# Kernel tuning notes

Hardware: AMD Instinct MI355X
Metric: run time of the kernel (lower is better)

The kernel has to match this reference:

```python
import jax, jax.numpy as jnp
import numpy as np

C = 128      # in channels
CO = 64      # out channels
G = 32       # group-norm groups
RES_IN = 32  # input resolution
RES_OUT = 64 # subdivided resolution
N = 20000    # active input voxels
EPS = 1e-5


def setup_inputs() -> dict:
    key = jax.random.key(0)
    ks = jax.random.split(key, 12)
    # unique active voxel coords at RES_IN (batch index 0, single instance)
    rng = np.random.default_rng(0)
    flat = rng.choice(RES_IN ** 3, size=N, replace=False)
    xyz = np.stack([flat // (RES_IN * RES_IN), (flat // RES_IN) % RES_IN, flat % RES_IN], axis=1)
    x_coords = jnp.asarray(np.concatenate([np.zeros((N, 1), np.int32), xyz.astype(np.int32)], axis=1))
    x_feats = jax.random.normal(ks[0], (N, C), dtype=jnp.float32)
    gn1_g = 1.0 + 0.1 * jax.random.normal(ks[1], (C,), dtype=jnp.float32)
    gn1_b = 0.1 * jax.random.normal(ks[2], (C,), dtype=jnp.float32)
    W1 = 0.05 * jax.random.normal(ks[3], (3, 3, 3, C, CO), dtype=jnp.float32)
    b1 = 0.01 * jax.random.normal(ks[4], (CO,), dtype=jnp.float32)
    gn2_g = 1.0 + 0.1 * jax.random.normal(ks[5], (CO,), dtype=jnp.float32)
    gn2_b = 0.1 * jax.random.normal(ks[6], (CO,), dtype=jnp.float32)
    W2 = 0.05 * jax.random.normal(ks[7], (3, 3, 3, CO, CO), dtype=jnp.float32)  # zero_module in source; random here to exercise math
    b2 = 0.01 * jax.random.normal(ks[8], (CO,), dtype=jnp.float32)
    Ws = 0.05 * jax.random.normal(ks[9], (C, CO), dtype=jnp.float32)   # 1x1 skip conv
    bs = 0.01 * jax.random.normal(ks[10], (CO,), dtype=jnp.float32)
    return dict(x_feats=x_feats, x_coords=x_coords, gn1_g=gn1_g, gn1_b=gn1_b,
                W1=W1, b1=b1, gn2_g=gn2_g, gn2_b=gn2_b, W2=W2, b2=b2, Ws=Ws, bs=bs)


def group_norm(f, g, b):
    # single-instance sparse group norm: stats per group over all points
    n, c = f.shape
    x = f.reshape(n, G, c // G)
    mu = jnp.mean(x, axis=(0, 2), keepdims=True)
    var = jnp.mean((x - mu) ** 2, axis=(0, 2), keepdims=True)
    return ((x - mu) * jax.lax.rsqrt(var + EPS)).reshape(n, c) * g + b


def subdivide(coords, feats):
    n = coords.shape[0]
    offs = jnp.stack(jnp.meshgrid(jnp.arange(2), jnp.arange(2), jnp.arange(2), indexing='ij'), -1).reshape(8, 3)
    xyz = coords[:, None, 1:] * 2 + offs[None].astype(coords.dtype)          # [n,8,3]
    bidx = jnp.broadcast_to(coords[:, None, :1], (n, 8, 1))
    new_coords = jnp.concatenate([bidx, xyz], axis=-1).reshape(n * 8, 4)
    return new_coords, jnp.repeat(feats, 8, axis=0)


def subm_conv3(coords, feats, W, b):
    # submanifold 3x3x3 sparse conv: scatter to padded dense grid, gather 27 neighbors per active site
    cin = feats.shape[1]
    grid = jnp.zeros((RES_OUT + 2, RES_OUT + 2, RES_OUT + 2, cin), feats.dtype)
    grid = grid.at[coords[:, 1] + 1, coords[:, 2] + 1, coords[:, 3] + 1].set(feats)
    acc = jnp.zeros((feats.shape[0], W.shape[-1]), feats.dtype)
    for i in range(3):
        for j in range(3):
            for k in range(3):
                nb = grid[coords[:, 1] + i, coords[:, 2] + j, coords[:, 3] + k]  # [n, cin]
                acc = acc + nb @ W[i, j, k]
    return acc + b


def reference(x_feats, x_coords, gn1_g, gn1_b, W1, b1, gn2_g, gn2_b, W2, b2, Ws, bs):
    h = jax.nn.silu(group_norm(x_feats, gn1_g, gn1_b))
    hc, hf = subdivide(x_coords, h)
    _, xf = subdivide(x_coords, x_feats)
    hf = subm_conv3(hc, hf, W1, b1)
    hf = jax.nn.silu(group_norm(hf, gn2_g, gn2_b))
    hf = subm_conv3(hc, hf, W2, b2)
    out = hf + (xf @ Ws + bs)  # residual + 1x1 skip conv (out_channels != channels)
    return out
```

## Files before the change

### kernel.cpp

```cpp
#include <hip/hip_runtime.h>
#include <hip/hip_bf16.h>
#include <math.h>

#define N_PTS 20000
#define C_IN 128
#define C_OUT 64
#define M_PTS (N_PTS*8)
#define EPS 1e-5f

typedef __attribute__((ext_vector_type(8))) short short8;
typedef __attribute__((ext_vector_type(4))) float float4v;

__device__ __forceinline__ ushort f2bf(float f){
    unsigned int i = __float_as_uint(f);
    unsigned int r = i + 0x7fffu + ((i >> 16) & 1u);
    return (ushort)(r >> 16);
}
__device__ __forceinline__ float bf2f(ushort u){ return __uint_as_float(((unsigned int)u) << 16); }
__device__ __forceinline__ float silu(float z){ return z / (1.f + expf(-z)); }


__global__ void __launch_bounds__(256) prep_kernel(
    const float* __restrict__ W1, const float* __restrict__ W2,
    ushort* __restrict__ Wt1, ushort* __restrict__ Wt2,
    int* __restrict__ pg, ushort* __restrict__ h, ushort* __restrict__ h2,
    const float* __restrict__ x, float* __restrict__ stats)
{
    const int b = blockIdx.x, tid = threadIdx.x;
    if (b < 864){
        int idx = b * 256 + tid;
        int j = idx & 7, l = (idx >> 3) & 63, nb = (idx >> 9) & 3, kb = (idx >> 11) & 3, t = idx >> 13;
        int ci = kb * 32 + (l >> 4) * 8 + j, co = nb * 16 + (l & 15);
        Wt1[idx] = f2bf(W1[(t * C_IN + ci) * 64 + co]);
    } else if (b < 1296){
        int idx = (b - 864) * 256 + tid;
        int j = idx & 7, l = (idx >> 3) & 63, nb = (idx >> 9) & 3, kb = (idx >> 11) & 1, t = idx >> 12;
        int ci = kb * 32 + (l >> 4) * 8 + j, co = nb * 16 + (l & 15);
        Wt2[idx] = f2bf(W2[(t * C_OUT + ci) * 64 + co]);
    } else if (b < 1424){
        int i = (b - 1296) * 256 + tid;
        pg[i] = -1;
        if (b == 1296){
            if (tid < C_IN) h[(size_t)N_PTS * C_IN + tid] = 0;
            if (tid < C_OUT) h2[(size_t)M_PTS * C_OUT + tid] = 0;
        }
    } else {
        __shared__ float ls[64];
        if (tid < 64) ls[tid] = 0.f;
        __syncthreads();
        const int g = tid & 31;
        const int r0 = (b - 1424) * 8 + (tid >> 5);
        float sum = 0.f, sq = 0.f;
        for (int r = r0; r < N_PTS; r += 4096){
            float4 v = *(const float4*)(x + (size_t)r * C_IN + g * 4);
            sum += v.x + v.y + v.z + v.w;
            sq  += v.x*v.x + v.y*v.y + v.z*v.z + v.w*v.w;
        }
        atomicAdd(&ls[g], sum);
        atomicAdd(&ls[32 + g], sq);
        __syncthreads();
        if (tid < 64) atomicAdd(&stats[tid], ls[tid]);
    }
}

__global__ void __launch_bounds__(256) mid_kernel(
    const int* __restrict__ cds, int* __restrict__ pg,
    const float* __restrict__ x, const float* __restrict__ stats,
    const float* __restrict__ g1, const float* __restrict__ b1, ushort* __restrict__ h,
    const float* __restrict__ Wsk, const float* __restrict__ bsk, float* __restrict__ s)
{
    __shared__ float w[C_IN * C_OUT];
    const int b = blockIdx.x, tid = threadIdx.x;
    if (b < 79){
        int i = b * 256 + tid;
        if (i < N_PTS){
            const int* cd = cds + i * 4;
            pg[(cd[1] * 32 + cd[2]) * 32 + cd[3]] = i;
        }
    } else if (b < 2579){
        int i = ((b - 79) * 256 + tid) * 4;
        int c0 = i & (C_IN - 1);
        int g = c0 >> 2;
        float mu = stats[g] * (1.0f / (N_PTS * 4.0f));
        float var = stats[32 + g] * (1.0f / (N_PTS * 4.0f)) - mu * mu;
        float rs = rsqrtf(var + EPS);
        float4 v = *(const float4*)(x + i);
        ushort4 o;
        o.x = f2bf(silu((v.x - mu) * rs * g1[c0+0] + b1[c0+0]));
        o.y = f2bf(silu((v.y - mu) * rs * g1[c0+1] + b1[c0+1]));
        o.z = f2bf(silu((v.z - mu) * rs * g1[c0+2] + b1[c0+2]));
        o.w = f2bf(silu((v.w - mu) * rs * g1[c0+3] + b1[c0+3]));
        *(ushort4*)(h + i) = o;
    } else {
        for (int j = tid; j < C_IN * C_OUT; j += 256) w[j] = Wsk[j];
        __syncthreads();
        int co = tid & 63, pr = tid >> 6;
        int p = (b - 2579) * 4 + pr;
        const float* xr = x + (size_t)p * C_IN;
        float a = bsk[co];
        for (int cb = 0; cb < C_IN; cb += 4){
            float4 v = *(const float4*)(xr + cb);
            a += v.x * w[(cb+0)*64+co] + v.y * w[(cb+1)*64+co]
               + v.z * w[(cb+2)*64+co] + v.w * w[(cb+3)*64+co];
        }
        s[(size_t)p * C_OUT + co] = a;
    }
}

template<int CIN, int CHILD>
__global__ void __launch_bounds__(64, 3) conv_direct(
    const ushort* __restrict__ feat, const int* __restrict__ pg,
    const int* __restrict__ coords, const ushort* __restrict__ Wt,
    const float* __restrict__ bias, const float* __restrict__ skip,
    ushort* __restrict__ hf1_bf, float* __restrict__ out, float* __restrict__ statsAcc)
{
    constexpr int KB = CIN / 32;
    __shared__ int rws[64];
    const int l = threadIdx.x;
    const int r16 = l & 15, qd = l >> 4;
    const int mb = blockIdx.x * 64;

    int cx0, cy0, cz0;
    {
        int m = mb + l, p = m >> 3, o = m & 7;
        cx0 = 2 * coords[p*4+1] + ((o >> 2) & 1);
        cy0 = 2 * coords[p*4+2] + ((o >> 1) & 1);
        cz0 = 2 * coords[p*4+3] + (o & 1);
    }

    float4v acc[4][4];
#pragma unroll
    for (int rb = 0; rb < 4; rb++)
#pragma unroll
        for (int nb = 0; nb < 4; nb++)
#pragma unroll
            for (int rg = 0; rg < 4; rg++) acc[rb][nb][rg] = 0.f;

    for (int t = 0; t < 27; t++){
        const int dx = t / 9 - 1, dy = (t / 3) % 3 - 1, dz = t % 3 - 1;
        const int cx = cx0 + dx, cy = cy0 + dy, cz = cz0 + dz;
        int row = 8 * N_PTS;
        if ((unsigned)cx < 64u && (unsigned)cy < 64u && (unsigned)cz < 64u){
            int pidx = pg[((cx >> 1) * 32 + (cy >> 1)) * 32 + (cz >> 1)];
            if (pidx >= 0) row = pidx * 8 + (((cx & 1) << 2) | ((cy & 1) << 1) | (cz & 1));
        }
        rws[l] = row;
        __syncthreads();
        int fr0 = rws[r16], fr1 = rws[16 + r16], fr2 = rws[32 + r16], fr3 = rws[48 + r16];
        if (!CHILD){ fr0 >>= 3; fr1 >>= 3; fr2 >>= 3; fr3 >>= 3; }
        const ushort* a0 = feat + (size_t)fr0 * CIN + qd * 8;
        const ushort* a1 = feat + (size_t)fr1 * CIN + qd * 8;
        const ushort* a2 = feat + (size_t)fr2 * CIN + qd * 8;
        const ushort* a3 = feat + (size_t)fr3 * CIN + qd * 8;
        const ushort* wt = Wt + (size_t)t * (KB * 2048) + l * 8;
#pragma unroll
        for (int kb = 0; kb < KB; kb++){
            short8 b0 = *(const short8*)(wt + (kb*4+0)*512);
            short8 b1 = *(const short8*)(wt + (kb*4+1)*512);
            short8 b2 = *(const short8*)(wt + (kb*4+2)*512);
            short8 b3 = *(const short8*)(wt + (kb*4+3)*512);
            short8 av0 = *(const short8*)(a0 + kb*32);
            short8 av1 = *(const short8*)(a1 + kb*32);
            short8 av2 = *(const short8*)(a2 + kb*32);
            short8 av3 = *(const short8*)(a3 + kb*32);
            acc[0][0] = __builtin_amdgcn_mfma_f32_16x16x32_bf16(av0, b0, acc[0][0], 0, 0, 0);
            acc[0][1] = __builtin_amdgcn_mfma_f32_16x16x32_bf16(av0, b1, acc[0][1], 0, 0, 0);
            acc[0][2] = __builtin_amdgcn_mfma_f32_16x16x32_bf16(av0, b2, acc[0][2], 0, 0, 0);
            acc[0][3] = __builtin_amdgcn_mfma_f32_16x16x32_bf16(av0, b3, acc[0][3], 0, 0, 0);
            acc[1][0] = __builtin_amdgcn_mfma_f32_16x16x32_bf16(av1, b0, acc[1][0], 0, 0, 0);
            acc[1][1] = __builtin_amdgcn_mfma_f32_16x16x32_bf16(av1, b1, acc[1][1], 0, 0, 0);
            acc[1][2] = __builtin_amdgcn_mfma_f32_16x16x32_bf16(av1, b2, acc[1][2], 0, 0, 0);
            acc[1][3] = __builtin_amdgcn_mfma_f32_16x16x32_bf16(av1, b3, acc[1][3], 0, 0, 0);
            acc[2][0] = __builtin_amdgcn_mfma_f32_16x16x32_bf16(av2, b0, acc[2][0], 0, 0, 0);
            acc[2][1] = __builtin_amdgcn_mfma_f32_16x16x32_bf16(av2, b1, acc[2][1], 0, 0, 0);
            acc[2][2] = __builtin_amdgcn_mfma_f32_16x16x32_bf16(av2, b2, acc[2][2], 0, 0, 0);
            acc[2][3] = __builtin_amdgcn_mfma_f32_16x16x32_bf16(av2, b3, acc[2][3], 0, 0, 0);
            acc[3][0] = __builtin_amdgcn_mfma_f32_16x16x32_bf16(av3, b0, acc[3][0], 0, 0, 0);
            acc[3][1] = __builtin_amdgcn_mfma_f32_16x16x32_bf16(av3, b1, acc[3][1], 0, 0, 0);
            acc[3][2] = __builtin_amdgcn_mfma_f32_16x16x32_bf16(av3, b2, acc[3][2], 0, 0, 0);
            acc[3][3] = __builtin_amdgcn_mfma_f32_16x16x32_bf16(av3, b3, acc[3][3], 0, 0, 0);
        }
    }

    float bsv[4] = { bias[r16], bias[16 + r16], bias[32 + r16], bias[48 + r16] };
    if (!CHILD){
        float ps[4] = {0,0,0,0}, pq[4] = {0,0,0,0};
#pragma unroll
        for (int rb = 0; rb < 4; rb++)
#pragma unroll
            for (int nb = 0; nb < 4; nb++)
#pragma unroll
                for (int rg = 0; rg < 4; rg++){
                    int mm = mb + rb * 16 + qd * 4 + rg;
                    float v = acc[rb][nb][rg] + bsv[nb];
                    hf1_bf[(size_t)mm * 64 + nb * 16 + r16] = f2bf(v);
                    ps[nb] += v; pq[nb] += v * v;
                }
#pragma unroll
        for (int nb = 0; nb < 4; nb++){
            float s1 = ps[nb], s2 = pq[nb];
            s1 += __shfl_xor(s1, 16, 64); s2 += __shfl_xor(s2, 16, 64);
            s1 += __shfl_xor(s1, 32, 64); s2 += __shfl_xor(s2, 32, 64);
            if (qd == 0){
                atomicAdd(&statsAcc[64 + nb * 16 + r16], s1);
                atomicAdd(&statsAcc[128 + nb * 16 + r16], s2);
            }
        }
    } else {
#pragma unroll
        for (int rb = 0; rb < 4; rb++)
#pragma unroll
            for (int rg = 0; rg < 4; rg++){
                int mm = mb + rb * 16 + qd * 4 + rg;
                const float* sk = skip + (size_t)(mm >> 3) * 64;
#pragma unroll
                for (int nb = 0; nb < 4; nb++){
                    int co = nb * 16 + r16;
                    out[(size_t)mm * 64 + co] = acc[rb][nb][rg] + bsv[nb] + sk[co];
                }
            }
    }
}

__global__ void __launch_bounds__(256) h2_kernel(
    const ushort* __restrict__ hf1, const float* __restrict__ stats,
    const float* __restrict__ gg, const float* __restrict__ gb, ushort* __restrict__ h2)
{
    int i = (blockIdx.x * 256 + threadIdx.x) * 4;
    if (i >= M_PTS * C_OUT) return;
    int c0 = i & (C_OUT - 1);
    const float inv = 1.0f / (M_PTS * 2.0f);
    float muA = (stats[64 + c0] + stats[64 + c0 + 1]) * inv;
    float vA  = (stats[128 + c0] + stats[128 + c0 + 1]) * inv - muA * muA;
    float rsA = rsqrtf(vA + EPS);
    float muB = (stats[64 + c0 + 2] + stats[64 + c0 + 3]) * inv;
    float vB  = (stats[128 + c0 + 2] + stats[128 + c0 + 3]) * inv - muB * muB;
    float rsB = rsqrtf(vB + EPS);
    ushort4 u = *(const ushort4*)(hf1 + i);
    ushort4 o;
    o.x = f2bf(silu((bf2f(u.x) - muA) * rsA * gg[c0+0] + gb[c0+0]));
    o.y = f2bf(silu((bf2f(u.y) - muA) * rsA * gg[c0+1] + gb[c0+1]));
    o.z = f2bf(silu((bf2f(u.z) - muB) * rsB * gg[c0+2] + gb[c0+2]));
    o.w = f2bf(silu((bf2f(u.w) - muB) * rsB * gg[c0+3] + gb[c0+3]));
    *(ushort4*)(h2 + i) = o;
}

extern "C" void kernel_launch(void* const* d_in, const int* in_sizes, int n_in,
                              void* d_out, int out_size, void* d_ws, size_t ws_size,
                              hipStream_t stream){
    const float* x   = (const float*)d_in[0];
    const int*   cds = (const int*)  d_in[1];
    const float* g1  = (const float*)d_in[2];
    const float* b1  = (const float*)d_in[3];
    const float* W1  = (const float*)d_in[4];
    const float* bb1 = (const float*)d_in[5];
    const float* g2  = (const float*)d_in[6];
    const float* b2  = (const float*)d_in[7];
    const float* W2  = (const float*)d_in[8];
    const float* bb2 = (const float*)d_in[9];
    const float* Wsk = (const float*)d_in[10];
    const float* bsk = (const float*)d_in[11];
    float* out = (float*)d_out;
    char* ws = (char*)d_ws;

    float*  stats = (float*) (ws);
    int*    pg    = (int*)   (ws + 1024);
    ushort* h     = (ushort*)(ws + 132096);
    ushort* h2    = (ushort*)(ws + 5252352);
    float*  s     = (float*) (ws + 25732480);
    ushort* Wt1   = (ushort*)(ws + 30852480);
    ushort* Wt2   = (ushort*)(ws + 31294848);

    hipMemsetAsync(stats, 0, 192 * sizeof(float), stream);
    prep_kernel<<<1936, 256, 0, stream>>>(W1, W2, Wt1, Wt2, pg, h, h2, x, stats);
    mid_kernel<<<7579, 256, 0, stream>>>(cds, pg, x, stats, g1, b1, h, Wsk, bsk, s);
    conv_direct<C_IN, 0><<<2500, 64, 0, stream>>>(h, pg, cds, Wt1, bb1, nullptr,
                                                  (ushort*)d_out, nullptr, stats);
    h2_kernel<<<12500, 256, 0, stream>>>((const ushort*)d_out, stats, g2, b2, h2);
    conv_direct<C_OUT, 1><<<2500, 64, 0, stream>>>(h2, pg, cds, Wt2, bb2, s,
                                                   nullptr, out, nullptr);
}
```

Measured before the change: 390.7 us.

## Fold conv1 taps by child parity into 8 summed parent weights

Because children of a voxel share duplicated features, the first conv's 27 taps collapse per child parity into 8 parent-neighbor taps with pre-summed weights. Conv1 now gathers parent rows (128 ch) with 8 taps instead of 27 per child, cutting MFMA work and gather traffic. Both convs also move to 32-row tiles with precomputed neighbor index tables in shared memory and a two-stage software-pipelined load/MFMA loop, replacing the per-tap barrier. The weight prep kernel grows to build the summed weights, and the summed weights are rounded to bf16 after summation.

```diff
diff --git a/kernel.cpp b/kernel.cpp
--- a/kernel.cpp
+++ b/kernel.cpp
@@ -19,28 +19,50 @@
 __device__ __forceinline__ float bf2f(ushort u){ return __uint_as_float(((unsigned int)u) << 16); }
 __device__ __forceinline__ float silu(float z){ return z / (1.f + expf(-z)); }
 
+struct Frag { short8 a0, a1, b0, b1, b2, b3; };
+
 
 __global__ void __launch_bounds__(256) prep_kernel(
     const float* __restrict__ W1, const float* __restrict__ W2,
-    ushort* __restrict__ Wt1, ushort* __restrict__ Wt2,
+    ushort* __restrict__ Wsum1, ushort* __restrict__ Wt2,
     int* __restrict__ pg, ushort* __restrict__ h, ushort* __restrict__ h2,
     const float* __restrict__ x, float* __restrict__ stats)
 {
     const int b = blockIdx.x, tid = threadIdx.x;
-    if (b < 864){
+    if (b < 2048){
         int idx = b * 256 + tid;
-        int j = idx & 7, l = (idx >> 3) & 63, nb = (idx >> 9) & 3, kb = (idx >> 11) & 3, t = idx >> 13;
-        int ci = kb * 32 + (l >> 4) * 8 + j, co = nb * 16 + (l & 15);
-        Wt1[idx] = f2bf(W1[(t * C_IN + ci) * 64 + co]);
-    } else if (b < 1296){
-        int idx = (b - 864) * 256 + tid;
-        int j = idx & 7, l = (idx >> 3) & 63, nb = (idx >> 9) & 3, kb = (idx >> 11) & 1, t = idx >> 12;
-        int ci = kb * 32 + (l >> 4) * 8 + j, co = nb * 16 + (l & 15);
+        int j = idx & 7, lq = (idx >> 3) & 63, nb = (idx >> 9) & 3, kb = (idx >> 11) & 3, tq = idx >> 13;
+        int o = tq >> 3, qi = tq & 7;
+        int bx = (o >> 2) & 1, by = (o >> 1) & 1, bz = o & 1;
+        int qx = (bx ? ((qi >> 2) & 1) : ((qi >> 2) & 1) - 1);
+        int qy = (by ? ((qi >> 1) & 1) : ((qi >> 1) & 1) - 1);
+        int qz = (bz ? (qi & 1) : (qi & 1) - 1);
+        int ci = kb * 32 + (lq >> 4) * 8 + j, co = nb * 16 + (lq & 15);
+        float sum = 0.f;
+#pragma unroll
+        for (int dx = -1; dx <= 1; dx++){
+            if (((bx + dx) >> 1) != qx) continue;
+#pragma unroll
+            for (int dy = -1; dy <= 1; dy++){
+                if (((by + dy) >> 1) != qy) continue;
+#pragma unroll
+                for (int dz = -1; dz <= 1; dz++){
+                    if (((bz + dz) >> 1) != qz) continue;
+                    int t = (dx + 1) * 9 + (dy + 1) * 3 + (dz + 1);
+                    sum += W1[(t * C_IN + ci) * 64 + co];
+                }
+            }
+        }
+        Wsum1[idx] = f2bf(sum);
+    } else if (b < 2480){
+        int idx = (b - 2048) * 256 + tid;
+        int j = idx & 7, lq = (idx >> 3) & 63, nb = (idx >> 9) & 3, kb = (idx >> 11) & 1, t = idx >> 12;
+        int ci = kb * 32 + (lq >> 4) * 8 + j, co = nb * 16 + (lq & 15);
         Wt2[idx] = f2bf(W2[(t * C_OUT + ci) * 64 + co]);
-    } else if (b < 1424){
-        int i = (b - 1296) * 256 + tid;
+    } else if (b < 2608){
+        int i = (b - 2480) * 256 + tid;
         pg[i] = -1;
-        if (b == 1296){
+        if (b == 2480){
             if (tid < C_IN) h[(size_t)N_PTS * C_IN + tid] = 0;
             if (tid < C_OUT) h2[(size_t)M_PTS * C_OUT + tid] = 0;
         }
@@ -49,7 +71,7 @@
         if (tid < 64) ls[tid] = 0.f;
         __syncthreads();
         const int g = tid & 31;
-        const int r0 = (b - 1424) * 8 + (tid >> 5);
+        const int r0 = (b - 2608) * 8 + (tid >> 5);
         float sum = 0.f, sq = 0.f;
         for (int r = r0; r < N_PTS; r += 4096){
             float4 v = *(const float4*)(x + (size_t)r * C_IN + g * 4);
@@ -107,119 +129,189 @@
     }
 }
 
-template<int CIN, int CHILD>
-__global__ void __launch_bounds__(64, 3) conv_direct(
+#define MFMA_STAGE(F) \
+    acc[0][0] = __builtin_amdgcn_mfma_f32_16x16x32_bf16(F.a0, F.b0, acc[0][0], 0, 0, 0); \
+    acc[0][1] = __builtin_amdgcn_mfma_f32_16x16x32_bf16(F.a0, F.b1, acc[0][1], 0, 0, 0); \
+    acc[0][2] = __builtin_amdgcn_mfma_f32_16x16x32_bf16(F.a0, F.b2, acc[0][2], 0, 0, 0); \
+    acc[0][3] = __builtin_amdgcn_mfma_f32_16x16x32_bf16(F.a0, F.b3, acc[0][3], 0, 0, 0); \
+    acc[1][0] = __builtin_amdgcn_mfma_f32_16x16x32_bf16(F.a1, F.b0, acc[1][0], 0, 0, 0); \
+    acc[1][1] = __builtin_amdgcn_mfma_f32_16x16x32_bf16(F.a1, F.b1, acc[1][1], 0, 0, 0); \
+    acc[1][2] = __builtin_amdgcn_mfma_f32_16x16x32_bf16(F.a1, F.b2, acc[1][2], 0, 0, 0); \
+    acc[1][3] = __builtin_amdgcn_mfma_f32_16x16x32_bf16(F.a1, F.b3, acc[1][3], 0, 0, 0);
+
+__global__ void __launch_bounds__(64, 4) conv1_parity(
+    const ushort* __restrict__ h, const int* __restrict__ pg,
+    const int* __restrict__ coords, const ushort* __restrict__ Wsum,
+    const float* __restrict__ bias, ushort* __restrict__ hf1_bf,
+    float* __restrict__ statsAcc)
+{
+    __shared__ int rws[8][32];
+    const int l = threadIdx.x;
+    const int r16 = l & 15, qd = l >> 4;
+    const int pb = blockIdx.x >> 3, o = blockIdx.x & 7;
+    const int bx = (o >> 2) & 1, by = (o >> 1) & 1, bz = o & 1;
+
+    if (l < 32){
+        int p = pb * 32 + l;
+        int px = 0, py = 0, pz = 0;
+        bool pv = p < N_PTS;
+        if (pv){ px = coords[p*4+1]; py = coords[p*4+2]; pz = coords[p*4+3]; }
+#pragma unroll
+        for (int qi = 0; qi < 8; qi++){
+            int nx = px + (bx ? ((qi >> 2) & 1) : ((qi >> 2) & 1) - 1);
+            int ny = py + (by ? ((qi >> 1) & 1) : ((qi >> 1) & 1) - 1);
+            int nz = pz + (bz ? (qi & 1) : (qi & 1) - 1);
+            int row = N_PTS;
+            if (pv && (unsigned)nx < 32u && (unsigned)ny < 32u && (unsigned)nz < 32u){
+                int pi = pg[(nx * 32 + ny) * 32 + nz];
+                if (pi >= 0) row = pi;
+            }
+            rws[qi][l] = row;
+        }
+    }
+    __syncthreads();
+
+    const ushort* wbase = Wsum + (size_t)o * 65536 + l * 8;
+    const int aoff = qd * 8;
+
+    float4v acc[2][4];
+#pragma unroll
+    for (int i = 0; i < 2; i++)
+#pragma unroll
+        for (int nb = 0; nb < 4; nb++)
+#pragma unroll
+            for (int rg = 0; rg < 4; rg++) acc[i][nb][rg] = 0.f;
+
+    auto LD = [&](int s, Frag& f){
+        int tap = s >> 2, kb = s & 3;
+        int fr0 = rws[tap][r16], fr1 = rws[tap][16 + r16];
+        const ushort* a0p = h + (size_t)fr0 * C_IN + aoff + kb * 32;
+        const ushort* a1p = h + (size_t)fr1 * C_IN + aoff + kb * 32;
+        const ushort* bp = wbase + (tap * 16 + kb * 4) * 512;
+        f.a0 = *(const short8*)a0p;
+        f.a1 = *(const short8*)a1p;
+        f.b0 = *(const short8*)(bp);
+        f.b1 = *(const short8*)(bp + 512);
+        f.b2 = *(const short8*)(bp + 1024);
+        f.b3 = *(const short8*)(bp + 1536);
+    };
+
+    Frag f0, f1;
+    LD(0, f0); LD(1, f1);
+#pragma unroll 2
+    for (int s = 0; s < 32; s++){
+        Frag nx;
+        if (s + 2 < 32) LD(s + 2, nx);
+        MFMA_STAGE(f0);
+        f0 = f1; f1 = nx;
+    }
+
+    float bsv[4] = { bias[r16], bias[16 + r16], bias[32 + r16], bias[48 + r16] };
+    float ps[4] = {0,0,0,0}, pq[4] = {0,0,0,0};
+#pragma unroll
+    for (int rb = 0; rb < 2; rb++)
+#pragma unroll
+        for (int rg = 0; rg < 4; rg++){
+            int p = pb * 32 + rb * 16 + qd * 4 + rg;
+            if (p < N_PTS){
+                size_t base = ((size_t)p * 8 + o) * 64;
+#pragma unroll
+                for (int nb = 0; nb < 4; nb++){
+                    float v = acc[rb][nb][rg] + bsv[nb];
+                    hf1_bf[base + nb * 16 + r16] = f2bf(v);
+                    ps[nb] += v; pq[nb] += v * v;
+                }
+            }
+        }
+#pragma unroll
+    for (int nb = 0; nb < 4; nb++){
+        float s1 = ps[nb], s2 = pq[nb];
+        s1 += __shfl_xor(s1, 16, 64); s2 += __shfl_xor(s2, 16, 64);
+        s1 += __shfl_xor(s1, 32, 64); s2 += __shfl_xor(s2, 32, 64);
+        if (qd == 0){
+            atomicAdd(&statsAcc[64 + nb * 16 + r16], s1);
+            atomicAdd(&statsAcc[128 + nb * 16 + r16], s2);
+        }
+    }
+}
+
+__global__ void __launch_bounds__(64, 4) conv2_direct(
     const ushort* __restrict__ feat, const int* __restrict__ pg,
     const int* __restrict__ coords, const ushort* __restrict__ Wt,
     const float* __restrict__ bias, const float* __restrict__ skip,
-    ushort* __restrict__ hf1_bf, float* __restrict__ out, float* __restrict__ statsAcc)
-{
-    constexpr int KB = CIN / 32;
-    __shared__ int rws[64];
+    float* __restrict__ out)
+{
+    __shared__ int rws[27][32];
     const int l = threadIdx.x;
     const int r16 = l & 15, qd = l >> 4;
-    const int mb = blockIdx.x * 64;
-
-    int cx0, cy0, cz0;
-    {
-        int m = mb + l, p = m >> 3, o = m & 7;
-        cx0 = 2 * coords[p*4+1] + ((o >> 2) & 1);
-        cy0 = 2 * coords[p*4+2] + ((o >> 1) & 1);
-        cz0 = 2 * coords[p*4+3] + (o & 1);
-    }
-
-    float4v acc[4][4];
-#pragma unroll
-    for (int rb = 0; rb < 4; rb++)
+    const int mb = blockIdx.x * 32;
+
+    if (l < 32){
+        int m = mb + l, p = m >> 3, oo = m & 7;
+        int cx0 = 2 * coords[p*4+1] + ((oo >> 2) & 1);
+        int cy0 = 2 * coords[p*4+2] + ((oo >> 1) & 1);
+        int cz0 = 2 * coords[p*4+3] + (oo & 1);
+#pragma unroll
+        for (int t = 0; t < 27; t++){
+            int cx = cx0 + t / 9 - 1, cy = cy0 + (t / 3) % 3 - 1, cz = cz0 + t % 3 - 1;
+            int row = M_PTS;
+            if ((unsigned)cx < 64u && (unsigned)cy < 64u && (unsigned)cz < 64u){
+                int pi = pg[((cx >> 1) * 32 + (cy >> 1)) * 32 + (cz >> 1)];
+                if (pi >= 0) row = pi * 8 + (((cx & 1) << 2) | ((cy & 1) << 1) | (cz & 1));
+            }
+            rws[t][l] = row;
+        }
+    }
+    __syncthreads();
+
+    const ushort* wbase = Wt + l * 8;
+    const int aoff = qd * 8;
+
+    float4v acc[2][4];
+#pragma unroll
+    for (int i = 0; i < 2; i++)
 #pragma unroll
         for (int nb = 0; nb < 4; nb++)
 #pragma unroll
-            for (int rg = 0; rg < 4; rg++) acc[rb][nb][rg] = 0.f;
-
-    for (int t = 0; t < 27; t++){
-        const int dx = t / 9 - 1, dy = (t / 3) % 3 - 1, dz = t % 3 - 1;
-        const int cx = cx0 + dx, cy = cy0 + dy, cz = cz0 + dz;
-        int row = 8 * N_PTS;
-        if ((unsigned)cx < 64u && (unsigned)cy < 64u && (unsigned)cz < 64u){
-            int pidx = pg[((cx >> 1) * 32 + (cy >> 1)) * 32 + (cz >> 1)];
-            if (pidx >= 0) row = pidx * 8 + (((cx & 1) << 2) | ((cy & 1) << 1) | (cz & 1));
-        }
-        rws[l] = row;
-        __syncthreads();
-        int fr0 = rws[r16], fr1 = rws[16 + r16], fr2 = rws[32 + r16], fr3 = rws[48 + r16];
-        if (!CHILD){ fr0 >>= 3; fr1 >>= 3; fr2 >>= 3; fr3 >>= 3; }
-        const ushort* a0 = feat + (size_t)fr0 * CIN + qd * 8;
-        const ushort* a1 = feat + (size_t)fr1 * CIN + qd * 8;
-        const ushort* a2 = feat + (size_t)fr2 * CIN + qd * 8;
-        const ushort* a3 = feat + (size_t)fr3 * CIN + qd * 8;
-        const ushort* wt = Wt + (size_t)t * (KB * 2048) + l * 8;
-#pragma unroll
-        for (int kb = 0; kb < KB; kb++){
-            short8 b0 = *(const short8*)(wt + (kb*4+0)*512);
-            short8 b1 = *(const short8*)(wt + (kb*4+1)*512);
-            short8 b2 = *(const short8*)(wt + (kb*4+2)*512);
-            short8 b3 = *(const short8*)(wt + (kb*4+3)*512);
-            short8 av0 = *(const short8*)(a0 + kb*32);
-            short8 av1 = *(const short8*)(a1 + kb*32);
-            short8 av2 = *(const short8*)(a2 + kb*32);
-            short8 av3 = *(const short8*)(a3 + kb*32);
-            acc[0][0] = __builtin_amdgcn_mfma_f32_16x16x32_bf16(av0, b0, acc[0][0], 0, 0, 0);
-            acc[0][1] = __builtin_amdgcn_mfma_f32_16x16x32_bf16(av0, b1, acc[0][1], 0, 0, 0);
-            acc[0][2] = __builtin_amdgcn_mfma_f32_16x16x32_bf16(av0, b2, acc[0][2], 0, 0, 0);
-            acc[0][3] = __builtin_amdgcn_mfma_f32_16x16x32_bf16(av0, b3, acc[0][3], 0, 0, 0);
-            acc[1][0] = __builtin_amdgcn_mfma_f32_16x16x32_bf16(av1, b0, acc[1][0], 0, 0, 0);
-            acc[1][1] = __builtin_amdgcn_mfma_f32_16x16x32_bf16(av1, b1, acc[1][1], 0, 0, 0);
-            acc[1][2] = __builtin_amdgcn_mfma_f32_16x16x32_bf16(av1, b2, acc[1][2], 0, 0, 0);
-            acc[1][3] = __builtin_amdgcn_mfma_f32_16x16x32_bf16(av1, b3, acc[1][3], 0, 0, 0);
-            acc[2][0] = __builtin_amdgcn_mfma_f32_16x16x32_bf16(av2, b0, acc[2][0], 0, 0, 0);
-            acc[2][1] = __builtin_amdgcn_mfma_f32_16x16x32_bf16(av2, b1, acc[2][1], 0, 0, 0);
-            acc[2][2] = __builtin_amdgcn_mfma_f32_16x16x32_bf16(av2, b2, acc[2][2], 0, 0, 0);
-            acc[2][3] = __builtin_amdgcn_mfma_f32_16x16x32_bf16(av2, b3, acc[2][3], 0, 0, 0);
-            acc[3][0] = __builtin_amdgcn_mfma_f32_16x16x32_bf16(av3, b0, acc[3][0], 0, 0, 0);
-            acc[3][1] = __builtin_amdgcn_mfma_f32_16x16x32_bf16(av3, b1, acc[3][1], 0, 0, 0);
-            acc[3][2] = __builtin_amdgcn_mfma_f32_16x16x32_bf16(av3, b2, acc[3][2], 0, 0, 0);
-            acc[3][3] = __builtin_amdgcn_mfma_f32_16x16x32_bf16(av3, b3, acc[3][3], 0, 0, 0);
-        }
+            for (int rg = 0; rg < 4; rg++) acc[i][nb][rg] = 0.f;
+
+    auto LD = [&](int s, Frag& f){
+        int tap = s >> 1, kb = s & 1;
+        int fr0 = rws[tap][r16], fr1 = rws[tap][16 + r16];
+        const ushort* a0p = feat + (size_t)fr0 * C_OUT + aoff + kb * 32;
+        const ushort* a1p = feat + (size_t)fr1 * C_OUT + aoff + kb * 32;
+        const ushort* bp = wbase + ((tap * 2 + kb) * 4) * 512;
+        f.a0 = *(const short8*)a0p;
+        f.a1 = *(const short8*)a1p;
+        f.b0 = *(const short8*)(bp);
+        f.b1 = *(const short8*)(bp + 512);
+        f.b2 = *(const short8*)(bp + 1024);
+        f.b3 = *(const short8*)(bp + 1536);
+    };
+
+    Frag f0, f1;
+    LD(0, f0); LD(1, f1);
+#pragma unroll 2
+    for (int s = 0; s < 54; s++){
+        Frag nx;
+        if (s + 2 < 54) LD(s + 2, nx);
+        MFMA_STAGE(f0);
+        f0 = f1; f1 = nx;
     }
 
     float bsv[4] = { bias[r16], bias[16 + r16], bias[32 + r16], bias[48 + r16] };
-    if (!CHILD){
-        float ps[4] = {0,0,0,0}, pq[4] = {0,0,0,0};
-#pragma unroll
-        for (int rb = 0; rb < 4; rb++)
-#pragma unroll
-            for (int nb = 0; nb < 4; nb++)
-#pragma unroll
-                for (int rg = 0; rg < 4; rg++){
-                    int mm = mb + rb * 16 + qd * 4 + rg;
-                    float v = acc[rb][nb][rg] + bsv[nb];
-                    hf1_bf[(size_t)mm * 64 + nb * 16 + r16] = f2bf(v);
-                    ps[nb] += v; pq[nb] += v * v;
-                }
-#pragma unroll
-        for (int nb = 0; nb < 4; nb++){
-            float s1 = ps[nb], s2 = pq[nb];
-            s1 += __shfl_xor(s1, 16, 64); s2 += __shfl_xor(s2, 16, 64);
-            s1 += __shfl_xor(s1, 32, 64); s2 += __shfl_xor(s2, 32, 64);
-            if (qd == 0){
-                atomicAdd(&statsAcc[64 + nb * 16 + r16], s1);
-                atomicAdd(&statsAcc[128 + nb * 16 + r16], s2);
-            }
-        }
-    } else {
-#pragma unroll
-        for (int rb = 0; rb < 4; rb++)
-#pragma unroll
-            for (int rg = 0; rg < 4; rg++){
-                int mm = mb + rb * 16 + qd * 4 + rg;
-                const float* sk = skip + (size_t)(mm >> 3) * 64;
-#pragma unroll
-                for (int nb = 0; nb < 4; nb++){
-                    int co = nb * 16 + r16;
-                    out[(size_t)mm * 64 + co] = acc[rb][nb][rg] + bsv[nb] + sk[co];
-                }
-            }
-    }
+#pragma unroll
+    for (int rb = 0; rb < 2; rb++)
+#pragma unroll
+        for (int rg = 0; rg < 4; rg++){
+            int mm = mb + rb * 16 + qd * 4 + rg;
+            const float* sk = skip + (size_t)(mm >> 3) * 64;
+#pragma unroll
+            for (int nb = 0; nb < 4; nb++){
+                int co = nb * 16 + r16;
+                out[(size_t)mm * 64 + co] = acc[rb][nb][rg] + bsv[nb] + sk[co];
+            }
+        }
 }
 
 __global__ void __launch_bounds__(256) h2_kernel(
@@ -268,15 +360,13 @@
     ushort* h     = (ushort*)(ws + 132096);
     ushort* h2    = (ushort*)(ws + 5252352);
     float*  s     = (float*) (ws + 25732480);
-    ushort* Wt1   = (ushort*)(ws + 30852480);
-    ushort* Wt2   = (ushort*)(ws + 31294848);
+    ushort* Wsum1 = (ushort*)(ws + 30852480);
+    ushort* Wt2   = (ushort*)(ws + 31901056);
 
     hipMemsetAsync(stats, 0, 192 * sizeof(float), stream);
-    prep_kernel<<<1936, 256, 0, stream>>>(W1, W2, Wt1, Wt2, pg, h, h2, x, stats);
+    prep_kernel<<<3120, 256, 0, stream>>>(W1, W2, Wsum1, Wt2, pg, h, h2, x, stats);
     mid_kernel<<<7579, 256, 0, stream>>>(cds, pg, x, stats, g1, b1, h, Wsk, bsk, s);
-    conv_direct<C_IN, 0><<<2500, 64, 0, stream>>>(h, pg, cds, Wt1, bb1, nullptr,
-                                                  (ushort*)d_out, nullptr, stats);
+    conv1_parity<<<625 * 8, 64, 0, stream>>>(h, pg, cds, Wsum1, bb1, (ushort*)d_out, stats);
     h2_kernel<<<12500, 256, 0, stream>>>((const ushort*)d_out, stats, g2, b2, h2);
-    conv_direct<C_OUT, 1><<<2500, 64, 0, stream>>>(h2, pg, cds, Wt2, bb2, s,
-                                                   nullptr, out, nullptr);
-}
+    conv2_direct<<<5000, 64, 0, stream>>>(h2, pg, cds, Wt2, bb2, s, out);
+}
```

Result: slower. 504.2 us (+29.0%).
